# Performance work log

Hardware: AMD Instinct MI355X
Metric: run time of the kernel (lower is better)

Reference implementation:

```python
import jax, jax.numpy as jnp
import numpy as np

N_NODES = 100000
N_EDGES = 2000000


def _init_mlp(key, dims, scale=0.05):
    Ws, bs = [], []
    ks = jax.random.split(key, len(dims) - 1)
    for k, di, do in zip(ks, dims[:-1], dims[1:]):
        Ws.append(jax.random.normal(k, (di, do), dtype=jnp.float32) * scale)
        bs.append(jnp.zeros((do,), dtype=jnp.float32))
    return Ws, bs


def setup_inputs() -> dict:
    key = jax.random.key(0)
    ks = jax.random.split(key, 7)
    d = {
        "t": jax.random.uniform(ks[0], (1,), dtype=jnp.float32),
        "x": jax.random.normal(ks[1], (N_NODES, 4), dtype=jnp.float32),
        "Ofixed": jax.random.normal(ks[2], (N_NODES, 2), dtype=jnp.float32),
        "src_idx": jax.random.randint(ks[3], (N_EDGES,), 0, N_NODES, dtype=jnp.int32),
        "tgt_idx": jax.random.randint(ks[4], (N_EDGES,), 0, N_NODES, dtype=jnp.int32),
    }
    # fR: (2*d_O+1)=13 -> [150]*4 -> 50 ; fO: 50 -> [100] -> 4
    R_Ws, R_bs = _init_mlp(ks[5], [13, 150, 150, 150, 150, 50])
    O_Ws, O_bs = _init_mlp(ks[6], [50, 100, 4])
    for i, (W, b) in enumerate(zip(R_Ws, R_bs)):
        d[f"fR_W{i}"] = W
        d[f"fR_b{i}"] = b
    for i, (W, b) in enumerate(zip(O_Ws, O_bs)):
        d[f"fO_W{i}"] = W
        d[f"fO_b{i}"] = b
    return d


def _mlp(h, Ws, bs):
    # hidden layers with ReLU, linear output (matches MLP in the torch code)
    for W, b in zip(Ws[:-1], bs[:-1]):
        h = jax.nn.relu(h @ W + b)
    return h @ Ws[-1] + bs[-1]


def reference(t, x, Ofixed, src_idx, tgt_idx,
              fR_W0, fR_b0, fR_W1, fR_b1, fR_W2, fR_b2, fR_W3, fR_b3, fR_W4, fR_b4,
              fO_W0, fO_b0, fO_W1, fO_b1):
    O = jnp.concatenate([x, Ofixed], axis=1)            # [N, d_O]
    # Msrc.T @ O and Mtgt.T @ O with 0/1 incidence matrices == gathers
    Rsrc = O[src_idx]                                   # [M, d_O]
    Rtgt = O[tgt_idx]                                   # [M, d_O]
    tt = jnp.broadcast_to(t.reshape(1, 1).astype(O.dtype), (src_idx.shape[0], 1))
    R_prime = jnp.concatenate([Rsrc, Rtgt, tt], axis=1)  # [M, 2*d_O+1]
    E = _mlp(R_prime, [fR_W0, fR_W1, fR_W2, fR_W3, fR_W4],
             [fR_b0, fR_b1, fR_b2, fR_b3, fR_b4])        # [M, d_E]
    # Mtgt @ E == scatter-add of edge messages onto target nodes
    E_prime = jax.ops.segment_sum(E, tgt_idx, num_segments=x.shape[0])  # [N, d_E]
    P = _mlp(E_prime, [fO_W0, fO_W1], [fO_b0, fO_b1])    # [N, d_P]
    return P
```

## Files before the change

### kernel.cpp

```cpp
#include <hip/hip_runtime.h>
#include <hip/hip_bf16.h>

typedef unsigned short u16;
typedef unsigned int u32;
typedef __attribute__((ext_vector_type(8))) short short8;
typedef __attribute__((ext_vector_type(4))) float f32x4;

constexpr int SA     = 160;
constexpr int BLK_E  = 128;
constexpr int NTHR   = 256;
constexpr int CHUNK  = 512;
constexpr int WSLOT  = 50 * CHUNK;
constexpr size_t WS_HDR   = 262144;

constexpr int Ls (int s) { return s == 0 ? 0 : (s <= 15 ? 1 + (s - 1) / 5 : 4); }
constexpr int Kss(int s) { return s == 0 ? 0 : (s <= 15 ? (s - 1) % 5 : s - 16); }

__device__ __forceinline__ u16 f2bf(float f) {
    union { float f; unsigned u; } c; c.f = f;
    return (u16)((c.u + 0x7fffu + ((c.u >> 16) & 1u)) >> 16);
}
__device__ __forceinline__ unsigned pk_bf16(float a, float b) {
    float2 f; f.x = a; f.y = b;
    __hip_bfloat162 h = __float22bfloat162_rn(f);
    return *(unsigned*)&h;
}

__device__ __forceinline__ int kperm(int kp) {
    if (kp < 64)  return (kp & 3) * 16 + (kp >> 2);
    if (kp < 128) { const int m = kp - 64; return (5 + (m & 3)) * 16 + (m >> 2); }
    if (kp < 144) return 4 * 16 + (kp - 128);
    if (kp < 160) return 9 * 16 + (kp - 144);
    return 1 << 30;
}

__global__ void prep_all(const float* __restrict__ W0, const float* __restrict__ W1,
                         const float* __restrict__ W2, const float* __restrict__ W3,
                         const float* __restrict__ W4,
                         const float* __restrict__ B0, const float* __restrict__ B1,
                         const float* __restrict__ B2, const float* __restrict__ B3,
                         const float* __restrict__ B4,
                         u16* __restrict__ Wt, u32* __restrict__ cursor, int n_nodes)
{
    const int l = blockIdx.y;
    if (l == 5) {
        for (int idx = blockIdx.x * blockDim.x + threadIdx.x; idx < n_nodes;
             idx += gridDim.x * blockDim.x)
            cursor[idx] = 0u;
        return;
    }
    const float* W; const float* B; int DI, DO; bool perm;
    if      (l == 0) { W = W0; B = B0; DI = 13;  DO = 150; perm = false; }
    else if (l == 1) { W = W1; B = B1; DI = 150; DO = 150; perm = true;  }
    else if (l == 2) { W = W2; B = B2; DI = 150; DO = 150; perm = true;  }
    else if (l == 3) { W = W3; B = B3; DI = 150; DO = 150; perm = true;  }
    else             { W = W4; B = B4; DI = 150; DO = 50;  perm = true;  }
    const int kbias = (l == 0) ? 13 : 150;
    u16* dst = Wt + (size_t)l * WSLOT;
    for (int idx = blockIdx.x * blockDim.x + threadIdx.x; idx < WSLOT;
         idx += gridDim.x * blockDim.x) {
        const int chunk = idx / CHUNK;
        const int within = idx - chunk * CHUNK;
        const int lane = within >> 3, e = within & 7;
        const int ks = chunk / 10, j = chunk - ks * 10;
        const int c = lane & 15, q = lane >> 4;
        const int n = j * 16 + c;
        const int kphys = ks * 32 + q * 8 + e;
        const int klog = perm ? kperm(kphys) : kphys;
        float v = 0.f;
        if (n < DO) {
            if (klog < DI)          v = W[klog * DO + n];
            else if (klog == kbias) v = B[n];
        }
        dst[idx] = f2bf(v);
    }
}

__device__ __forceinline__ void loadHalfH(const u16* __restrict__ Wt, int h,
                                          int lane, short8* buf)
{
    int l, ks, g, nch;
    if (h < 32) { const int s = h >> 1; l = Ls(s); ks = Kss(s); g = h & 1; nch = 5; }
    else        { l = 4; ks = h - 32; g = 0; nch = 4; }
    const u16* base = Wt + (size_t)l * WSLOT + (size_t)(ks * 10 + g * 5) * CHUNK
                         + lane * 8;
#pragma unroll
    for (int jj = 0; jj < 5; ++jj)
        if (jj < nch) buf[jj] = *(const short8*)&base[jj * CHUNK];
}

__device__ __forceinline__ void epilogueF(u16* act, int ebase, int col, int quad,
                                          f32x4 (&acc)[2][10])
{
#pragma unroll
    for (int mtl = 0; mtl < 2; ++mtl)
#pragma unroll
        for (int r = 0; r < 4; ++r) {
            const int row = ebase + mtl * 16 + quad * 4 + r;
            u16* rp = &act[row * SA];
            uint2 p0, p1;
            p0.x = pk_bf16(fmaxf(acc[mtl][0][r], 0.f), fmaxf(acc[mtl][1][r], 0.f));
            p0.y = pk_bf16(fmaxf(acc[mtl][2][r], 0.f), fmaxf(acc[mtl][3][r], 0.f));
            p1.x = pk_bf16(fmaxf(acc[mtl][5][r], 0.f), fmaxf(acc[mtl][6][r], 0.f));
            p1.y = pk_bf16(fmaxf(acc[mtl][7][r], 0.f), fmaxf(acc[mtl][8][r], 0.f));
            *(uint2*)&rp[col * 4]      = p0;
            *(uint2*)&rp[64 + col * 4] = p1;
            rp[128 + col] = (u16)pk_bf16(fmaxf(acc[mtl][4][r], 0.f), 0.f);
            u16 sv = (u16)pk_bf16(fmaxf(acc[mtl][9][r], 0.f), 0.f);
            if (col == 6) sv = 0x3F80;
            rp[144 + col] = sv;
        }
}

__global__ void hist_kernel(const int* __restrict__ tgt, u32* __restrict__ cnt,
                            int n_edges)
{
    const int e = blockIdx.x * blockDim.x + threadIdx.x;
    if (e < n_edges) atomicAdd(&cnt[tgt[e]], 1u);
}

__global__ void scan1_kernel(const u32* __restrict__ cnt, u32* __restrict__ offs,
                             u32* __restrict__ bsum, int n)
{
    __shared__ u32 s[256];
    const int i = blockIdx.x * 256 + threadIdx.x;
    const u32 v = (i < n) ? cnt[i] : 0u;
    s[threadIdx.x] = v; __syncthreads();
#pragma unroll
    for (int d = 1; d < 256; d <<= 1) {
        const u32 t = (threadIdx.x >= d) ? s[threadIdx.x - d] : 0u;
        __syncthreads();
        s[threadIdx.x] += t;
        __syncthreads();
    }
    if (i < n) offs[i] = s[threadIdx.x] - v;
    if (threadIdx.x == 255) bsum[blockIdx.x] = s[255];
}

__global__ void scan2_kernel(u32* __restrict__ bsum, int nb)
{
    __shared__ u32 s[512];
    const int i = threadIdx.x;
    const u32 v = (i < nb) ? bsum[i] : 0u;
    s[i] = v; __syncthreads();
#pragma unroll
    for (int d = 1; d < 512; d <<= 1) {
        const u32 t = (i >= d) ? s[i - d] : 0u;
        __syncthreads();
        s[i] += t;
        __syncthreads();
    }
    if (i < nb) bsum[i] = s[i] - v;
}

__global__ void scan3_kernel(u32* __restrict__ offs, const u32* __restrict__ bsum,
                             u32* __restrict__ cursor, int n, int n_edges)
{
    const int i = blockIdx.x * 256 + threadIdx.x;
    if (i < n) {
        const u32 o = offs[i] + bsum[blockIdx.x];
        offs[i] = o;
        cursor[i] = o;
    }
    if (blockIdx.x == 0 && threadIdx.x == 0) offs[n] = (u32)n_edges;
}

__global__ void perm_kernel(const int* __restrict__ src, const int* __restrict__ tgt,
                            u32* __restrict__ cursor, int2* __restrict__ sg,
                            int n_edges)
{
    const int e = blockIdx.x * blockDim.x + threadIdx.x;
    if (e < n_edges) {
        const int g = tgt[e];
        const u32 pos = atomicAdd(&cursor[g], 1u);
        sg[pos] = make_int2(src[e], g);
    }
}

__global__ __launch_bounds__(NTHR, 3) void edge_kernel(
    const float* __restrict__ t, const float* __restrict__ x, const float* __restrict__ Ofx,
    const int2* __restrict__ sgp,
    const u16* __restrict__ Wt,
    float* __restrict__ Ep, int n_edges)
{
    __shared__ __align__(16) u16 act[BLK_E * SA];

    const int tid   = threadIdx.x;
    const int lane  = tid & 63;
    const int wv    = tid >> 6;
    const int ebase = wv * 32;
    const int col   = lane & 15;
    const int quad  = lane >> 4;

    int gval = -1;
    if (lane < 32) {
        const int e = ebase + lane;
        const long long ge = (long long)blockIdx.x * BLK_E + e;
        const bool valid = ge < n_edges;
        const int2 sg = valid ? sgp[ge] : make_int2(0, 0);
        gval = valid ? sg.y : -1;
        const float4 xs = valid ? *(const float4*)&x[(size_t)sg.x * 4] : float4{0, 0, 0, 0};
        const float2 os = valid ? *(const float2*)&Ofx[(size_t)sg.x * 2] : float2{0, 0};
        const float4 xg = valid ? *(const float4*)&x[(size_t)sg.y * 4] : float4{0, 0, 0, 0};
        const float2 og = valid ? *(const float2*)&Ofx[(size_t)sg.y * 2] : float2{0, 0};
        const float tv = valid ? t[0] : 0.f;
        uint4 w0, w1;
        w0.x = pk_bf16(xs.x, xs.y); w0.y = pk_bf16(xs.z, xs.w);
        w0.z = pk_bf16(os.x, os.y); w0.w = pk_bf16(xg.x, xg.y);
        w1.x = pk_bf16(xg.z, xg.w); w1.y = pk_bf16(og.x, og.y);
        w1.z = pk_bf16(tv, 1.0f);   w1.w = 0u;
        u16* rp = &act[e * SA];
        *(uint4*)&rp[0]  = w0;
        *(uint4*)&rp[8]  = w1;
        *(uint4*)&rp[16] = uint4{0, 0, 0, 0};
        *(uint4*)&rp[24] = uint4{0, 0, 0, 0};
    }

    const f32x4 z = {0.f, 0.f, 0.f, 0.f};
    f32x4 acc[2][10];
    short8 Wb[2][5];
    short8 Af[2];

    loadHalfH(Wt, 0, lane, Wb[0]);
    loadHalfH(Wt, 1, lane, Wb[1]);

#pragma unroll
    for (int s = 0; s <= 15; ++s) {
        const int ks = Kss(s);
        const bool first = (s == 0) || (ks == 0);
#pragma unroll
        for (int mtl = 0; mtl < 2; ++mtl)
            Af[mtl] = *(const short8*)&act[(ebase + mtl * 16 + col) * SA
                                           + ks * 32 + quad * 8];
#pragma unroll
        for (int jj = 0; jj < 5; ++jj)
#pragma unroll
            for (int mtl = 0; mtl < 2; ++mtl)
                acc[mtl][jj] = __builtin_amdgcn_mfma_f32_16x16x32_bf16(
                    Af[mtl], Wb[0][jj], first ? z : acc[mtl][jj], 0, 0, 0);
        loadHalfH(Wt, 2 * s + 2, lane, Wb[0]);
#pragma unroll
        for (int jj = 0; jj < 5; ++jj)
#pragma unroll
            for (int mtl = 0; mtl < 2; ++mtl)
                acc[mtl][5 + jj] = __builtin_amdgcn_mfma_f32_16x16x32_bf16(
                    Af[mtl], Wb[1][jj], first ? z : acc[mtl][5 + jj], 0, 0, 0);
        loadHalfH(Wt, 2 * s + 3, lane, Wb[1]);
        if (s == 0 || ks == 4)
            epilogueF(act, ebase, col, quad, acc);
    }

    f32x4 acc4[2][4];
#pragma unroll
    for (int ks4 = 0; ks4 < 5; ++ks4) {
        const int h = 32 + ks4;
#pragma unroll
        for (int mtl = 0; mtl < 2; ++mtl)
            Af[mtl] = *(const short8*)&act[(ebase + mtl * 16 + col) * SA
                                           + ks4 * 32 + quad * 8];
#pragma unroll
        for (int jj = 0; jj < 4; ++jj)
#pragma unroll
            for (int mtl = 0; mtl < 2; ++mtl)
                acc4[mtl][jj] = __builtin_amdgcn_mfma_f32_16x16x32_bf16(
                    Af[mtl], Wb[h & 1][jj], (ks4 == 0) ? z : acc4[mtl][jj], 0, 0, 0);
        if (h + 2 <= 36) loadHalfH(Wt, h + 2, lane, Wb[h & 1]);
    }

    float* actF = (float*)&act[ebase * SA];
#pragma unroll
    for (int mtl = 0; mtl < 2; ++mtl)
#pragma unroll
        for (int jj = 0; jj < 4; ++jj) {
            const int n = jj * 16 + col;
            if (n < 50) {
#pragma unroll
                for (int r = 0; r < 4; ++r)
                    actF[(mtl * 16 + quad * 4 + r) * 52 + n] = acc4[mtl][jj][r];
            }
        }
    if (lane < 50) {
        const int c = lane;
        int   cur = __shfl(gval, 0);
        float a   = 0.f;
#pragma unroll
        for (int rb = 0; rb < 4; ++rb) {
            float vb[8];
#pragma unroll
            for (int j = 0; j < 8; ++j)
                vb[j] = actF[(rb * 8 + j) * 52 + c];
#pragma unroll
            for (int j = 0; j < 8; ++j) {
                const int g = __shfl(gval, rb * 8 + j);
                if (g != cur) {
                    if (cur >= 0) atomicAdd(&Ep[(size_t)cur * 50 + c], a);
                    a = 0.f; cur = g;
                }
                a += vb[j];
            }
        }
        if (cur >= 0) atomicAdd(&Ep[(size_t)cur * 50 + c], a);
    }
}

template<int DI, int DO, bool RELU>
__device__ __forceinline__ void mlp_layer_t(
    const float* __restrict__ W, const float* __restrict__ B,
    float (*in)[64], float (*out)[64], int tid)
{
    const int et = tid & 15;
    const int jt = tid >> 4;
    constexpr int NG = (DO + 15) / 16;

    float acc0[NG], acc1[NG], acc2[NG], acc3[NG];
#pragma unroll
    for (int g = 0; g < NG; ++g) {
        const int j = jt + 16 * g;
        const float bb = (j < DO) ? B[j] : 0.f;
        acc0[g] = bb; acc1[g] = bb; acc2[g] = bb; acc3[g] = bb;
    }
    for (int k = 0; k < DI; ++k) {
        const float4 a = *(const float4*)&in[k][et * 4];
#pragma unroll
        for (int g = 0; g < NG; ++g) {
            const int j = jt + 16 * g;
            const float wv = (j < DO) ? W[k * DO + j] : 0.f;
            acc0[g] = fmaf(a.x, wv, acc0[g]);
            acc1[g] = fmaf(a.y, wv, acc1[g]);
            acc2[g] = fmaf(a.z, wv, acc2[g]);
            acc3[g] = fmaf(a.w, wv, acc3[g]);
        }
    }
#pragma unroll
    for (int g = 0; g < NG; ++g) {
        const int j = jt + 16 * g;
        if (j < DO) {
            float4 v; v.x = acc0[g]; v.y = acc1[g]; v.z = acc2[g]; v.w = acc3[g];
            if (RELU) {
                v.x = fmaxf(v.x, 0.f); v.y = fmaxf(v.y, 0.f);
                v.z = fmaxf(v.z, 0.f); v.w = fmaxf(v.w, 0.f);
            }
            *(float4*)&out[j][et * 4] = v;
        }
    }
}

__global__ __launch_bounds__(256, 2) void node_kernel(
    const float* __restrict__ Ep,
    const float* __restrict__ W0, const float* __restrict__ B0,
    const float* __restrict__ W1, const float* __restrict__ B1,
    float* __restrict__ P, int n_nodes)
{
    __shared__ float bufA[104][64];
    __shared__ float bufB[104][64];
    const int tid = threadIdx.x;
    const int n0  = blockIdx.x * 64;

    for (int idx = tid; idx < 64 * 50; idx += 256) {
        const int e = idx / 50;
        const int k = idx - e * 50;
        const int n = n0 + e;
        bufA[k][e] = (n < n_nodes) ? Ep[(size_t)n * 50 + k] : 0.f;
    }
    __syncthreads();
    mlp_layer_t<50, 100, true >(W0, B0, bufA, bufB, tid); __syncthreads();
    mlp_layer_t<100, 4, false>(W1, B1, bufB, bufA, tid); __syncthreads();
    for (int idx = tid; idx < 64 * 4; idx += 256) {
        const int e = idx & 63;
        const int j = idx >> 6;
        const int n = n0 + e;
        if (n < n_nodes) P[(size_t)n * 4 + j] = bufA[j][e];
    }
}

extern "C" void kernel_launch(void* const* d_in, const int* in_sizes, int n_in,
                              void* d_out, int out_size, void* d_ws, size_t ws_size,
                              hipStream_t stream)
{
    const float* t   = (const float*)d_in[0];
    const float* x   = (const float*)d_in[1];
    const float* Ofx = (const float*)d_in[2];
    const int*   src = (const int*)d_in[3];
    const int*   tgt = (const int*)d_in[4];
    const float* W0  = (const float*)d_in[5];  const float* B0 = (const float*)d_in[6];
    const float* W1  = (const float*)d_in[7];  const float* B1 = (const float*)d_in[8];
    const float* W2  = (const float*)d_in[9];  const float* B2 = (const float*)d_in[10];
    const float* W3  = (const float*)d_in[11]; const float* B3 = (const float*)d_in[12];
    const float* W4  = (const float*)d_in[13]; const float* B4 = (const float*)d_in[14];
    const float* OW0 = (const float*)d_in[15]; const float* OB0 = (const float*)d_in[16];
    const float* OW1 = (const float*)d_in[17]; const float* OB1 = (const float*)d_in[18];

    const int n_nodes = in_sizes[1] / 4;
    const int n_edges = in_sizes[3];

    auto align256 = [](size_t v) { return (v + 255) & ~(size_t)255; };
    char* ws = (char*)d_ws;
    const size_t copy_elems = (size_t)n_nodes * 50;
    size_t o = 0;
    u16*   Wt       = (u16*)(ws + o);  o = WS_HDR;
    float* Ep       = (float*)(ws + o); o = align256(o + copy_elems * sizeof(float));
    u32*   offs     = (u32*)(ws + o);  o = align256(o + (size_t)(n_nodes + 1) * 4);
    u32*   cursor   = (u32*)(ws + o);  o = align256(o + (size_t)n_nodes * 4);
    u32*   bsum     = (u32*)(ws + o);  o = align256(o + 512 * 4);
    int2*  sg_perm  = (int2*)(ws + o); o = align256(o + (size_t)n_edges * 8);

    const int NB  = (n_nodes + 255) / 256;
    const int EBK = (n_edges + 255) / 256;

    prep_all<<<dim3(32, 6), 256, 0, stream>>>(W0, W1, W2, W3, W4,
                                              B0, B1, B2, B3, B4, Wt,
                                              cursor, n_nodes);
    hipMemsetAsync(Ep, 0, copy_elems * sizeof(float), stream);

    hist_kernel <<<EBK, 256, 0, stream>>>(tgt, cursor, n_edges);
    scan1_kernel<<<NB, 256, 0, stream>>>(cursor, offs, bsum, n_nodes);
    scan2_kernel<<<1, 512, 0, stream>>>(bsum, NB);
    scan3_kernel<<<NB, 256, 0, stream>>>(offs, bsum, cursor, n_nodes, n_edges);
    perm_kernel <<<EBK, 256, 0, stream>>>(src, tgt, cursor, sg_perm, n_edges);

    edge_kernel<<<(n_edges + BLK_E - 1) / BLK_E, NTHR, 0, stream>>>(
        t, x, Ofx, sg_perm, Wt, Ep, n_edges);

    node_kernel<<<(n_nodes + 63) / 64, 256, 0, stream>>>(
        Ep, OW0, OB0, OW1, OB1, (float*)d_out, n_nodes);
}
```

Measured before the change: 881.2 us.

## Store edge order indices, remap blocks per XCD, fold Ep zeroing into prep

The permutation kernel now writes a 4-byte edge index instead of an 8-byte (src,tgt) pair, and the edge kernel does an extra indirect load of src/tgt through that index. Edge-kernel block IDs are remapped so contiguous sorted-edge ranges land on the same XCD, aiming at better L2 locality for the segment scatter. The Ep memset is folded into the prep kernel as an extra grid row, and the node kernel's launch bound is raised to 3 blocks per CU. The extra indirection adds random reads in the edge kernel in exchange for less write traffic in perm.

```diff
diff --git a/kernel.cpp b/kernel.cpp
--- a/kernel.cpp
+++ b/kernel.cpp
@@ -40,13 +40,20 @@
                          const float* __restrict__ B0, const float* __restrict__ B1,
                          const float* __restrict__ B2, const float* __restrict__ B3,
                          const float* __restrict__ B4,
-                         u16* __restrict__ Wt, u32* __restrict__ cursor, int n_nodes)
+                         u16* __restrict__ Wt, u32* __restrict__ cursor, int n_nodes,
+                         float* __restrict__ Ep, int ep_quads)
 {
     const int l = blockIdx.y;
+    const int tid0 = blockIdx.x * blockDim.x + threadIdx.x;
+    const int stride = gridDim.x * blockDim.x;
     if (l == 5) {
-        for (int idx = blockIdx.x * blockDim.x + threadIdx.x; idx < n_nodes;
-             idx += gridDim.x * blockDim.x)
-            cursor[idx] = 0u;
+        for (int idx = tid0; idx < n_nodes; idx += stride) cursor[idx] = 0u;
+        return;
+    }
+    if (l == 6) {
+        float4* p = (float4*)Ep;
+        const float4 z4 = {0.f, 0.f, 0.f, 0.f};
+        for (int idx = tid0; idx < ep_quads; idx += stride) p[idx] = z4;
         return;
     }
     const float* W; const float* B; int DI, DO; bool perm;
@@ -57,8 +64,7 @@
     else             { W = W4; B = B4; DI = 150; DO = 50;  perm = true;  }
     const int kbias = (l == 0) ? 13 : 150;
     u16* dst = Wt + (size_t)l * WSLOT;
-    for (int idx = blockIdx.x * blockDim.x + threadIdx.x; idx < WSLOT;
-         idx += gridDim.x * blockDim.x) {
+    for (int idx = tid0; idx < WSLOT; idx += stride) {
         const int chunk = idx / CHUNK;
         const int within = idx - chunk * CHUNK;
         const int lane = within >> 3, e = within & 7;
@@ -153,37 +159,38 @@
     if (i < nb) bsum[i] = s[i] - v;
 }
 
-__global__ void scan3_kernel(u32* __restrict__ offs, const u32* __restrict__ bsum,
-                             u32* __restrict__ cursor, int n, int n_edges)
+__global__ void scan3_kernel(const u32* __restrict__ offs, const u32* __restrict__ bsum,
+                             u32* __restrict__ cursor, int n)
 {
     const int i = blockIdx.x * 256 + threadIdx.x;
-    if (i < n) {
-        const u32 o = offs[i] + bsum[blockIdx.x];
-        offs[i] = o;
-        cursor[i] = o;
-    }
-    if (blockIdx.x == 0 && threadIdx.x == 0) offs[n] = (u32)n_edges;
-}
-
-__global__ void perm_kernel(const int* __restrict__ src, const int* __restrict__ tgt,
-                            u32* __restrict__ cursor, int2* __restrict__ sg,
-                            int n_edges)
+    if (i < n) cursor[i] = offs[i] + bsum[blockIdx.x];
+}
+
+__global__ void perm_kernel(const int* __restrict__ tgt, u32* __restrict__ cursor,
+                            u32* __restrict__ ord, int n_edges)
 {
     const int e = blockIdx.x * blockDim.x + threadIdx.x;
     if (e < n_edges) {
-        const int g = tgt[e];
-        const u32 pos = atomicAdd(&cursor[g], 1u);
-        sg[pos] = make_int2(src[e], g);
+        const u32 pos = atomicAdd(&cursor[tgt[e]], 1u);
+        ord[pos] = (u32)e;
     }
 }
 
 __global__ __launch_bounds__(NTHR, 3) void edge_kernel(
     const float* __restrict__ t, const float* __restrict__ x, const float* __restrict__ Ofx,
-    const int2* __restrict__ sgp,
+    const u32* __restrict__ ordp,
+    const int* __restrict__ src, const int* __restrict__ tgt,
     const u16* __restrict__ Wt,
     float* __restrict__ Ep, int n_edges)
 {
     __shared__ __align__(16) u16 act[BLK_E * SA];
+
+    const int nwg  = gridDim.x;
+    const int orig = blockIdx.x;
+    const int xcd  = orig & 7;
+    const int q = nwg >> 3, r = nwg & 7;
+    const int bid = (xcd < r ? xcd * (q + 1) : r * (q + 1) + (xcd - r) * q)
+                    + (orig >> 3);
 
     const int tid   = threadIdx.x;
     const int lane  = tid & 63;
@@ -195,14 +202,17 @@
     int gval = -1;
     if (lane < 32) {
         const int e = ebase + lane;
-        const long long ge = (long long)blockIdx.x * BLK_E + e;
+        const long long ge = (long long)bid * BLK_E + e;
         const bool valid = ge < n_edges;
-        const int2 sg = valid ? sgp[ge] : make_int2(0, 0);
-        gval = valid ? sg.y : -1;
-        const float4 xs = valid ? *(const float4*)&x[(size_t)sg.x * 4] : float4{0, 0, 0, 0};
-        const float2 os = valid ? *(const float2*)&Ofx[(size_t)sg.x * 2] : float2{0, 0};
-        const float4 xg = valid ? *(const float4*)&x[(size_t)sg.y * 4] : float4{0, 0, 0, 0};
-        const float2 og = valid ? *(const float2*)&Ofx[(size_t)sg.y * 2] : float2{0, 0};
+        const u32 idx = valid ? ordp[ge] : 0u;
+        const int sidx = valid ? src[idx] : 0;
+        const int g    = valid ? tgt[idx] : -1;
+        gval = g;
+        const int gi = valid ? g : 0;
+        const float4 xs = valid ? *(const float4*)&x[(size_t)sidx * 4] : float4{0, 0, 0, 0};
+        const float2 os = valid ? *(const float2*)&Ofx[(size_t)sidx * 2] : float2{0, 0};
+        const float4 xg = valid ? *(const float4*)&x[(size_t)gi * 4] : float4{0, 0, 0, 0};
+        const float2 og = valid ? *(const float2*)&Ofx[(size_t)gi * 2] : float2{0, 0};
         const float tv = valid ? t[0] : 0.f;
         uint4 w0, w1;
         w0.x = pk_bf16(xs.x, xs.y); w0.y = pk_bf16(xs.z, xs.w);
@@ -345,7 +355,7 @@
     }
 }
 
-__global__ __launch_bounds__(256, 2) void node_kernel(
+__global__ __launch_bounds__(256, 3) void node_kernel(
     const float* __restrict__ Ep,
     const float* __restrict__ W0, const float* __restrict__ B0,
     const float* __restrict__ W1, const float* __restrict__ B1,
@@ -399,27 +409,27 @@
     size_t o = 0;
     u16*   Wt       = (u16*)(ws + o);  o = WS_HDR;
     float* Ep       = (float*)(ws + o); o = align256(o + copy_elems * sizeof(float));
-    u32*   offs     = (u32*)(ws + o);  o = align256(o + (size_t)(n_nodes + 1) * 4);
+    u32*   offs     = (u32*)(ws + o);  o = align256(o + (size_t)n_nodes * 4);
     u32*   cursor   = (u32*)(ws + o);  o = align256(o + (size_t)n_nodes * 4);
     u32*   bsum     = (u32*)(ws + o);  o = align256(o + 512 * 4);
-    int2*  sg_perm  = (int2*)(ws + o); o = align256(o + (size_t)n_edges * 8);
+    u32*   ord      = (u32*)(ws + o);  o = align256(o + (size_t)n_edges * 4);
 
     const int NB  = (n_nodes + 255) / 256;
     const int EBK = (n_edges + 255) / 256;
-
-    prep_all<<<dim3(32, 6), 256, 0, stream>>>(W0, W1, W2, W3, W4,
+    const int ep_quads = (int)(copy_elems / 4);
+
+    prep_all<<<dim3(64, 7), 256, 0, stream>>>(W0, W1, W2, W3, W4,
                                               B0, B1, B2, B3, B4, Wt,
-                                              cursor, n_nodes);
-    hipMemsetAsync(Ep, 0, copy_elems * sizeof(float), stream);
+                                              cursor, n_nodes, Ep, ep_quads);
 
     hist_kernel <<<EBK, 256, 0, stream>>>(tgt, cursor, n_edges);
     scan1_kernel<<<NB, 256, 0, stream>>>(cursor, offs, bsum, n_nodes);
     scan2_kernel<<<1, 512, 0, stream>>>(bsum, NB);
-    scan3_kernel<<<NB, 256, 0, stream>>>(offs, bsum, cursor, n_nodes, n_edges);
-    perm_kernel <<<EBK, 256, 0, stream>>>(src, tgt, cursor, sg_perm, n_edges);
+    scan3_kernel<<<NB, 256, 0, stream>>>(offs, bsum, cursor, n_nodes);
+    perm_kernel <<<EBK, 256, 0, stream>>>(tgt, cursor, ord, n_edges);
 
     edge_kernel<<<(n_edges + BLK_E - 1) / BLK_E, NTHR, 0, stream>>>(
-        t, x, Ofx, sg_perm, Wt, Ep, n_edges);
+        t, x, Ofx, ord, src, tgt, Wt, Ep, n_edges);
 
     node_kernel<<<(n_nodes + 63) / 64, 256, 0, stream>>>(
         Ep, OW0, OB0, OW1, OB1, (float*)d_out, n_nodes);
```

New measurement: 1.029 ms. 1.17x slower.
